# Performance work log

Hardware: AMD Instinct MI355X
Metric: run time of the kernel (lower is better)

Reference implementation:

```python
import jax, jax.numpy as jnp
import numpy as np
from functools import partial

B, N, T_HIST, T_FCST, HID, F, DEG = 16, 2000, 24, 24, 64, 8, 32
E_TOTAL = B * N * DEG


def setup_inputs() -> dict:
    key = jax.random.key(0)
    ks = jax.random.split(key, 20)
    s = 1.0 / np.sqrt(HID)
    # block-diagonal batched edge_index, as built by _process_adj_mat
    src = jax.random.randint(ks[0], (B, N * DEG), 0, N, dtype=jnp.int32)
    dst = jax.random.randint(ks[1], (B, N * DEG), 0, N, dtype=jnp.int32)
    off = (jnp.arange(B, dtype=jnp.int32) * N)[:, None]
    edge_index = jnp.stack([(src + off).reshape(-1), (dst + off).reshape(-1)], axis=0)
    return {
        "pm25_hist": jax.random.normal(ks[2], (B, T_HIST, N, 1), jnp.float32),
        "feature": jax.random.normal(ks[3], (B, T_HIST + T_FCST, N, F), jnp.float32),
        "edge_index": edge_index,
        "w_ih_enc": jax.random.normal(ks[4], (3 * HID, 2), jnp.float32) * s,
        "w_hh_enc": jax.random.normal(ks[5], (3 * HID, HID), jnp.float32) * s,
        "b_ih_enc": jnp.zeros((3 * HID,), jnp.float32),
        "b_hh_enc": jnp.zeros((3 * HID,), jnp.float32),
        "fc_w": jax.random.normal(ks[6], (1, HID), jnp.float32) * s,
        "fc_b": jnp.zeros((1,), jnp.float32),
        "cheb_w0": jax.random.normal(ks[7], (F + 1, 1), jnp.float32) * s,
        "cheb_w1": jax.random.normal(ks[8], (F + 1, 1), jnp.float32) * s,
        "cheb_b": jnp.zeros((1,), jnp.float32),
        "w_ih_dec": jax.random.normal(ks[9], (3 * HID, F + 2), jnp.float32) * s,
        "w_hh_dec": jax.random.normal(ks[10], (3 * HID, HID), jnp.float32) * s,
        "b_ih_dec": jnp.zeros((3 * HID,), jnp.float32),
        "b_hh_dec": jnp.zeros((3 * HID,), jnp.float32),
        "out_w": jax.random.normal(ks[11], (1, 2 * HID), jnp.float32) * s,
        "out_b": jnp.zeros((1,), jnp.float32),
    }


def gru(x, h, w_ih, w_hh, b_ih, b_hh):
    gi = x @ w_ih.T + b_ih
    gh = h @ w_hh.T + b_hh
    i_r, i_z, i_n = jnp.split(gi, 3, axis=-1)
    h_r, h_z, h_n = jnp.split(gh, 3, axis=-1)
    r = jax.nn.sigmoid(i_r + h_r)
    z = jax.nn.sigmoid(i_z + h_z)
    n = jnp.tanh(i_n + r * h_n)
    return (1.0 - z) * n + z * h


def cheb_conv(x, edge_index, w0, w1, b):
    # ChebConv K=2, sym norm, lambda_max=2 -> T1(L_hat) = -D^-1/2 A D^-1/2
    src, dst = edge_index[0], edge_index[1]
    ones = jnp.ones(src.shape, x.dtype)
    deg = jax.ops.segment_sum(ones, dst, num_segments=B * N)
    dis = jnp.where(deg > 0, jax.lax.rsqrt(jnp.maximum(deg, 1.0)), 0.0)
    norm = -(dis[src] * dis[dst])
    tx1 = jax.ops.segment_sum(norm[:, None] * x[src], dst, num_segments=B * N)
    return x @ w0 + tx1 @ w1 + b


def reference(pm25_hist, feature, edge_index, w_ih_enc, w_hh_enc, b_ih_enc, b_hh_enc,
              fc_w, fc_b, cheb_w0, cheb_w1, cheb_b, w_ih_dec, w_hh_dec, b_ih_dec,
              b_hh_dec, out_w, out_b):
    # ---------------- encoder ----------------
    h0 = jnp.zeros((B * N, HID), pm25_hist.dtype)
    x0 = jnp.zeros((B, N, 1), pm25_hist.dtype)

    def enc_step(carry, pm_t):
        hn, xn = carry
        x = jnp.concatenate([xn, pm_t], axis=-1).reshape(B * N, 2)
        hn = gru(x, hn, w_ih_enc, w_hh_enc, b_ih_enc, b_hh_enc)
        h3 = hn.reshape(B, N, HID)
        xn = h3 @ fc_w.T + fc_b
        return (hn, xn), h3

    (hn, xn), Hs = jax.lax.scan(enc_step, (h0, x0), pm25_hist.transpose(1, 0, 2, 3))
    H = Hs.transpose(1, 0, 2, 3)  # (B, T_HIST, N, HID)

    # ---------------- decoder ----------------
    def dec_step(carry, feat_t):
        hn, xn = carry
        x = jnp.concatenate([xn, feat_t], axis=-1)  # (B, N, F+1)
        xg = jax.nn.sigmoid(cheb_conv(x.reshape(B * N, F + 1), edge_index,
                                      cheb_w0, cheb_w1, cheb_b))
        x2 = jnp.concatenate([x, xg.reshape(B, N, 1)], axis=-1).reshape(B * N, F + 2)
        hn = gru(x2, hn, w_ih_dec, w_hh_dec, b_ih_dec, b_hh_dec)
        xn3 = hn.reshape(B, N, HID)
        energy = jnp.einsum('btnd,bnd->bnt', H, xn3)  # history attention
        alpha = jax.nn.softmax(energy, axis=2)
        a = jnp.einsum('bnt,btnd->bnd', alpha, H)
        xn = jnp.concatenate([a, xn3], axis=-1) @ out_w.T + out_b
        return (hn, xn), xn

    feats = feature[:, T_HIST:].transpose(1, 0, 2, 3)  # (T_FCST, B, N, F)
    _, preds = jax.lax.scan(dec_step, (hn, xn), feats)
    return preds.transpose(1, 0, 2, 3)  # (B, T_FCST, N, 1)
```

## Files before the change

kernel.cpp:

```cpp
#include <hip/hip_runtime.h>
#include <hip/hip_bf16.h>
#include <cstddef>
#include <cstdint>

constexpr int NB    = 16;
constexpr int NN    = 2000;
constexpr int TH    = 24;
constexpr int TF    = 24;
constexpr int HID   = 64;
constexpr int NF    = 8;
constexpr int NODES = NB * NN;
constexpr int ETOT  = NODES * 32;
constexpr int TT    = TH + TF;
constexpr int BLKN  = 64;
constexpr int NBLK  = NODES / BLKN;

typedef __attribute__((ext_vector_type(8))) short bf16x8;
typedef __attribute__((ext_vector_type(4))) float f32x4;
typedef uint16_t u16;

__device__ __forceinline__ float sigmoidf_(float x) { return 1.f / (1.f + __expf(-x)); }
__device__ __forceinline__ float tanhf_(float x) {
    float e = __expf(2.f * x);
    return 1.f - 2.f / (e + 1.f);
}
__device__ __forceinline__ u16 bfh(float x) {
    __hip_bfloat16 b = __float2bfloat16(x);
    u16 u; __builtin_memcpy(&u, &b, 2); return u;
}
__device__ __forceinline__ float bff(u16 u) { return __uint_as_float(((uint32_t)u) << 16); }
__device__ __forceinline__ uint32_t pk(u16 a, u16 b) { return (uint32_t)a | ((uint32_t)b << 16); }

__global__ void k_init(float* __restrict__ dis) {
    int i = blockIdx.x * blockDim.x + threadIdx.x;
    if (i < NODES) dis[i] = 0.f;
}

__global__ void k_deg(const int* __restrict__ ei, float* __restrict__ deg) {
    int e = blockIdx.x * blockDim.x + threadIdx.x;
    if (e < ETOT) atomicAdd(&deg[ei[ETOT + e]], 1.0f);
}

__global__ __launch_bounds__(256) void k_scan(const float* __restrict__ degf,
                                              int* __restrict__ row0,
                                              int* __restrict__ cnt)
{
    __shared__ int part[256];
    const int tid = threadIdx.x;
    const int per = NODES / 256;
    const int base = tid * per;
    int s = 0;
    for (int i = 0; i < per; i++) s += (int)degf[base + i];
    part[tid] = s;
    __syncthreads();
    for (int off = 1; off < 256; off <<= 1) {
        int v = (tid >= off) ? part[tid - off] : 0;
        __syncthreads();
        part[tid] += v;
        __syncthreads();
    }
    int run = (tid == 0) ? 0 : part[tid - 1];
    for (int i = 0; i < per; i++) {
        row0[base + i] = run;
        cnt[base + i]  = 0;
        run += (int)degf[base + i];
    }
    if (tid == 255) row0[NODES] = run;
}

__global__ void k_dis(float* __restrict__ dis) {
    int i = blockIdx.x * blockDim.x + threadIdx.x;
    if (i < NODES) {
        float d = dis[i];
        dis[i] = (d > 0.f) ? rsqrtf(fmaxf(d, 1.f)) : 0.f;
    }
}

__global__ void k_fill(const int* __restrict__ ei, const float* __restrict__ dis,
                       const int* __restrict__ row0, int* __restrict__ cnt,
                       int2* __restrict__ edge8)
{
    int e = blockIdx.x * blockDim.x + threadIdx.x;
    if (e < ETOT) {
        int s = ei[e];
        int d = ei[ETOT + e];
        float nv = -(dis[s] * dis[d]);
        int p = atomicAdd(&cnt[d], 1);
        edge8[row0[d] + p] = make_int2(s, __float_as_int(nv));
    }
}

__global__ void k_prepE(const float* __restrict__ whe, const float* __restrict__ fcw,
                        u16* __restrict__ AH, u16* __restrict__ AL)
{
    int i = blockIdx.x * blockDim.x + threadIdx.x;
    if (i < 208 * 64) {
        int r = i >> 6, k = i & 63;
        float v = (r < 192) ? whe[r * 64 + k] : ((r == 192) ? fcw[k] : 0.f);
        u16 hi = bfh(v);
        AH[i] = hi;
        AL[i] = bfh(v - bff(hi));
    }
}

__global__ void k_prepD(const float* __restrict__ whd, const float* __restrict__ wihd,
                        u16* __restrict__ AH, u16* __restrict__ AL)
{
    int i = blockIdx.x * blockDim.x + threadIdx.x;
    if (i < 256 * 96) {
        int r = i / 96, k = i - r * 96;
        float v = 0.f;
        if (k < 64) {
            if (r < 192) v = whd[r * 64 + k];
        } else if (k < 74) {
            int xi = k - 64;
            if (r < 128)       v = wihd[r * 10 + xi];
            else if (r >= 192) v = wihd[(r - 64) * 10 + xi];
        }
        u16 hi = bfh(v);
        AH[i] = hi;
        AL[i] = bfh(v - bff(hi));
    }
}

__global__ __launch_bounds__(256, 2) void k_encM(
    const float* __restrict__ pm, const u16* __restrict__ AeH, const u16* __restrict__ AeL,
    const float* __restrict__ w_ih, const float* __restrict__ b_ih, const float* __restrict__ b_hh,
    const float* __restrict__ fc_b, const float* __restrict__ feat, const float* __restrict__ cw1,
    u16* __restrict__ BgH, u16* __restrict__ BgL, u16* __restrict__ Hb,
    float* __restrict__ xn_buf, float* __restrict__ y1)
{
    __shared__ u16 BH[2][64 * 64], BL[2][64 * 64];
    __shared__ float pmL[TH * BLKN];
    __shared__ float xnL[BLKN];

    const int tid = threadIdx.x;
    const int l   = tid & 63;
    const int wv  = __builtin_amdgcn_readfirstlane(tid >> 6);
    const int n0  = blockIdx.x * BLKN;
    const int cn  = l & 15;
    const int kg  = l >> 4;
    const int c0  = wv * 16 + kg * 4;

    for (int i = tid; i < 64 * 64 / 2; i += 256) {
        ((uint32_t*)BH[0])[i] = 0u;
        ((uint32_t*)BL[0])[i] = 0u;
    }
    for (int i = tid; i < TH * BLKN; i += 256) {
        int t = i >> 6, n = i & 63;
        int node = n0 + n, b = node / NN, nn2 = node - b * NN;
        pmL[i] = pm[(b * TH + t) * NN + nn2];
    }
    bf16x8 AHf[4][2], ALf[4][2];
    #pragma unroll
    for (int s = 0; s < 4; s++) {
        #pragma unroll
        for (int ks = 0; ks < 2; ks++) {
            bf16x8 zh = {0,0,0,0,0,0,0,0};
            AHf[s][ks] = zh; ALf[s][ks] = zh;
            if (s < 3 || wv == 0) {
                int row = (wv + 4 * s) * 16 + cn;
                int off = row * 64 + ks * 32 + kg * 8;
                AHf[s][ks] = *(const bf16x8*)(AeH + off);
                ALf[s][ks] = *(const bf16x8*)(AeL + off);
            }
        }
    }
    float bR[4], bZ[4], biN[4], bhN[4];
    float wR0[4], wR1[4], wZ0[4], wZ1[4], wN0[4], wN1[4];
    #pragma unroll
    for (int j = 0; j < 4; j++) {
        int c = c0 + j;
        bR[j]  = b_ih[c] + b_hh[c];
        bZ[j]  = b_ih[64 + c] + b_hh[64 + c];
        biN[j] = b_ih[128 + c];
        bhN[j] = b_hh[128 + c];
        wR0[j] = w_ih[2 * c];           wR1[j] = w_ih[2 * c + 1];
        wZ0[j] = w_ih[2 * (64 + c)];    wZ1[j] = w_ih[2 * (64 + c) + 1];
        wN0[j] = w_ih[2 * (128 + c)];   wN1[j] = w_ih[2 * (128 + c) + 1];
    }
    const float fcb = fc_b[0];
    __syncthreads();

    for (int t = 0; t < TH; t++) {
        const int cur = t & 1, nxt = cur ^ 1;
        f32x4 acc[4][4];
        #pragma unroll
        for (int s = 0; s < 4; s++)
            #pragma unroll
            for (int ct = 0; ct < 4; ct++)
                acc[s][ct] = (f32x4){0.f, 0.f, 0.f, 0.f};

        #pragma unroll
        for (int ct = 0; ct < 4; ct++) {
            const int n = ct * 16 + cn;
            #pragma unroll
            for (int ks = 0; ks < 2; ks++) {
                const int idx = (n * 64 + ks * 32 + kg * 8) ^ ((n & 7) << 3);
                bf16x8 bh = *(const bf16x8*)&BH[cur][idx];
                bf16x8 bl = *(const bf16x8*)&BL[cur][idx];
                #pragma unroll
                for (int s = 0; s < 4; s++) {
                    if (s < 3 || wv == 0) {
                        acc[s][ct] = __builtin_amdgcn_mfma_f32_16x16x32_bf16(AHf[s][ks], bh, acc[s][ct], 0, 0, 0);
                        acc[s][ct] = __builtin_amdgcn_mfma_f32_16x16x32_bf16(AHf[s][ks], bl, acc[s][ct], 0, 0, 0);
                        acc[s][ct] = __builtin_amdgcn_mfma_f32_16x16x32_bf16(ALf[s][ks], bh, acc[s][ct], 0, 0, 0);
                    }
                }
            }
        }
        if (wv == 0 && kg == 0) {
            #pragma unroll
            for (int ct = 0; ct < 4; ct++) xnL[ct * 16 + cn] = acc[3][ct][0];
        }
        __syncthreads();

        #pragma unroll
        for (int ct = 0; ct < 4; ct++) {
            const int n = ct * 16 + cn, node = n0 + n;
            float xn = 0.f;
            if (t > 0) xn = xnL[n] + fcb;
            const float pv = pmL[t * 64 + n];
            const int hidx = (n * 64 + c0) ^ ((n & 7) << 3);
            uint2 oh = *(const uint2*)&BH[cur][hidx];
            uint2 ol = *(const uint2*)&BL[cur][hidx];
            float hnew[4];
            #pragma unroll
            for (int j = 0; j < 4; j++) {
                u16 hh = (j < 2) ? (u16)((j == 0) ? (oh.x & 0xffff) : (oh.x >> 16))
                                 : (u16)((j == 2) ? (oh.y & 0xffff) : (oh.y >> 16));
                u16 ll = (j < 2) ? (u16)((j == 0) ? (ol.x & 0xffff) : (ol.x >> 16))
                                 : (u16)((j == 2) ? (ol.y & 0xffff) : (ol.y >> 16));
                float hold = bff(hh) + bff(ll);
                float r  = sigmoidf_(acc[0][ct][j] + bR[j] + wR0[j] * xn + wR1[j] * pv);
                float z  = sigmoidf_(acc[1][ct][j] + bZ[j] + wZ0[j] * xn + wZ1[j] * pv);
                float gi = biN[j] + wN0[j] * xn + wN1[j] * pv;
                float gh = acc[2][ct][j] + bhN[j];
                float nn_ = tanhf_(gi + r * gh);
                hnew[j] = (1.f - z) * nn_ + z * hold;
            }
            u16 nh0 = bfh(hnew[0]), nh1 = bfh(hnew[1]), nh2 = bfh(hnew[2]), nh3 = bfh(hnew[3]);
            u16 nl0 = bfh(hnew[0] - bff(nh0)), nl1 = bfh(hnew[1] - bff(nh1));
            u16 nl2 = bfh(hnew[2] - bff(nh2)), nl3 = bfh(hnew[3] - bff(nh3));
            uint2 ph = make_uint2(pk(nh0, nh1), pk(nh2, nh3));
            uint2 pl = make_uint2(pk(nl0, nl1), pk(nl2, nl3));
            *(uint2*)&BH[nxt][hidx] = ph;
            *(uint2*)&BL[nxt][hidx] = pl;
            *(uint2*)(Hb + (size_t)node * (TH * HID) + t * HID + c0) = ph;
        }
        __syncthreads();
    }

    if (wv == 0) {
        f32x4 ax[4];
        #pragma unroll
        for (int ct = 0; ct < 4; ct++) ax[ct] = (f32x4){0.f, 0.f, 0.f, 0.f};
        #pragma unroll
        for (int ct = 0; ct < 4; ct++) {
            const int n = ct * 16 + cn;
            #pragma unroll
            for (int ks = 0; ks < 2; ks++) {
                const int idx = (n * 64 + ks * 32 + kg * 8) ^ ((n & 7) << 3);
                bf16x8 bh = *(const bf16x8*)&BH[0][idx];
                bf16x8 bl = *(const bf16x8*)&BL[0][idx];
                ax[ct] = __builtin_amdgcn_mfma_f32_16x16x32_bf16(AHf[3][ks], bh, ax[ct], 0, 0, 0);
                ax[ct] = __builtin_amdgcn_mfma_f32_16x16x32_bf16(AHf[3][ks], bl, ax[ct], 0, 0, 0);
                ax[ct] = __builtin_amdgcn_mfma_f32_16x16x32_bf16(ALf[3][ks], bh, ax[ct], 0, 0, 0);
            }
        }
        if (kg == 0) {
            #pragma unroll
            for (int ct = 0; ct < 4; ct++) xnL[ct * 16 + cn] = ax[ct][0];
        }
    }
    __syncthreads();

    for (int i = tid; i < 512; i += 256) {
        int n = i >> 3, sl = i & 7;
        int idx = (n * 64 + sl * 8) ^ ((n & 7) << 3);
        *(uint4*)(BgH + ((size_t)(n0 + n)) * 64 + sl * 8) = *(const uint4*)&BH[0][idx];
        *(uint4*)(BgL + ((size_t)(n0 + n)) * 64 + sl * 8) = *(const uint4*)&BL[0][idx];
    }
    if (tid < BLKN) {
        int n = tid, node = n0 + n;
        float xv = xnL[n] + fcb;
        xn_buf[node] = xv;
        int b = node / NN, nn2 = node - b * NN;
        const float* fp = feat + ((size_t)(b * TT + TH) * NN + nn2) * NF;
        float yy = xv * cw1[0];
        #pragma unroll
        for (int q = 0; q < NF; q++) yy += fp[q] * cw1[1 + q];
        y1[node] = yy;
    }
}

__global__ __launch_bounds__(256) void k_gather(
    const int* __restrict__ row0, const int2* __restrict__ edge8,
    const float* __restrict__ y1, float* __restrict__ tx)
{
    const int tid  = blockIdx.x * 256 + threadIdx.x;
    const int node = tid >> 2;
    const int q    = tid & 3;
    if (node >= NODES) return;
    const int beg = row0[node], end = row0[node + 1];
    float acc = 0.f;
    for (int i = beg + q; i < end; i += 4) {
        const int2 e = edge8[i];
        acc = fmaf(__int_as_float(e.y), y1[e.x], acc);
    }
    acc += __shfl_xor(acc, 1, 64);
    acc += __shfl_xor(acc, 2, 64);
    if (q == 0) tx[node] = acc;
}

__global__ __launch_bounds__(256, 2) void k_decM(
    const float* __restrict__ feat, const u16* __restrict__ AdH, const u16* __restrict__ AdL,
    const float* __restrict__ b_ih, const float* __restrict__ b_hh,
    const float* __restrict__ w0, const float* __restrict__ cb,
    const float* __restrict__ xn_buf, const float* __restrict__ tx,
    const u16* __restrict__ BgHin, const u16* __restrict__ BgLin,
    u16* __restrict__ BgHout, u16* __restrict__ BgLout, int t)
{
    __shared__ u16 XH[64 * 96], XL[64 * 96];
    const int tid = threadIdx.x;
    const int l   = tid & 63;
    const int wv  = __builtin_amdgcn_readfirstlane(tid >> 6);
    const int n0  = blockIdx.x * BLKN;
    const int cn  = l & 15, kg = l >> 4;
    const int c0  = wv * 16 + kg * 4;

    for (int i = tid; i < 512; i += 256) {
        int n = i >> 3, sl = i & 7;
        int idx = (n * 96 + sl * 8) ^ ((n & 7) << 3);
        *(uint4*)&XH[idx] = *(const uint4*)(BgHin + ((size_t)(n0 + n)) * 64 + sl * 8);
        *(uint4*)&XL[idx] = *(const uint4*)(BgLin + ((size_t)(n0 + n)) * 64 + sl * 8);
    }
    if (tid < BLKN) {
        int n = tid, node = n0 + n;
        int b = node / NN, nn2 = node - b * NN;
        float x0 = xn_buf[node];
        const float* fp = feat + ((size_t)(b * TT + TH + t) * NN + nn2) * NF;
        float f0 = fp[0], f1 = fp[1], f2 = fp[2], f3 = fp[3];
        float f4 = fp[4], f5 = fp[5], f6 = fp[6], f7 = fp[7];
        float xw = x0 * w0[0];
        xw = fmaf(f0, w0[1], xw); xw = fmaf(f1, w0[2], xw);
        xw = fmaf(f2, w0[3], xw); xw = fmaf(f3, w0[4], xw);
        xw = fmaf(f4, w0[5], xw); xw = fmaf(f5, w0[6], xw);
        xw = fmaf(f6, w0[7], xw); xw = fmaf(f7, w0[8], xw);
        float xg = sigmoidf_(xw + tx[node] + cb[0]);
        u16 h0 = bfh(x0), h1 = bfh(f0), h2 = bfh(f1), h3 = bfh(f2), h4 = bfh(f3);
        u16 h5 = bfh(f4), h6 = bfh(f5), h7 = bfh(f6), h8 = bfh(f7), h9 = bfh(xg);
        u16 l0 = bfh(x0 - bff(h0)), l1 = bfh(f0 - bff(h1)), l2 = bfh(f1 - bff(h2));
        u16 l3 = bfh(f2 - bff(h3)), l4 = bfh(f3 - bff(h4)), l5 = bfh(f4 - bff(h5));
        u16 l6 = bfh(f5 - bff(h6)), l7 = bfh(f6 - bff(h7)), l8 = bfh(f7 - bff(h8));
        u16 l9 = bfh(xg - bff(h9));
        uint4 qh0 = make_uint4(pk(h0, h1), pk(h2, h3), pk(h4, h5), pk(h6, h7));
        uint4 qh1 = make_uint4(pk(h8, h9), 0u, 0u, 0u);
        uint4 ql0 = make_uint4(pk(l0, l1), pk(l2, l3), pk(l4, l5), pk(l6, l7));
        uint4 ql1 = make_uint4(pk(l8, l9), 0u, 0u, 0u);
        uint4 zz  = make_uint4(0u, 0u, 0u, 0u);
        const int sw = (n & 7) << 3;
        *(uint4*)&XH[(n * 96 + 64) ^ sw] = qh0;
        *(uint4*)&XH[(n * 96 + 72) ^ sw] = qh1;
        *(uint4*)&XH[(n * 96 + 80) ^ sw] = zz;
        *(uint4*)&XH[(n * 96 + 88) ^ sw] = zz;
        *(uint4*)&XL[(n * 96 + 64) ^ sw] = ql0;
        *(uint4*)&XL[(n * 96 + 72) ^ sw] = ql1;
        *(uint4*)&XL[(n * 96 + 80) ^ sw] = zz;
        *(uint4*)&XL[(n * 96 + 88) ^ sw] = zz;
    }
    float bsR[4], bsZ[4], biN[4], bhN[4];
    #pragma unroll
    for (int j = 0; j < 4; j++) {
        int c = c0 + j;
        bsR[j] = b_ih[c] + b_hh[c];
        bsZ[j] = b_ih[64 + c] + b_hh[64 + c];
        biN[j] = b_ih[128 + c];
        bhN[j] = b_hh[128 + c];
    }
    bf16x8 AHf[4][3], ALf[4][3];
    #pragma unroll
    for (int s = 0; s < 4; s++) {
        #pragma unroll
        for (int ks = 0; ks < 3; ks++) {
            bf16x8 zh = {0,0,0,0,0,0,0,0};
            AHf[s][ks] = zh; ALf[s][ks] = zh;
            const bool live = (s < 2) || (s == 2 && ks < 2) || (s == 3 && ks == 2);
            if (live) {
                int row = (wv + 4 * s) * 16 + cn;
                int off = row * 96 + ks * 32 + kg * 8;
                AHf[s][ks] = *(const bf16x8*)(AdH + off);
                ALf[s][ks] = *(const bf16x8*)(AdL + off);
            }
        }
    }
    __syncthreads();

    f32x4 acc[4][4];
    #pragma unroll
    for (int s = 0; s < 4; s++)
        #pragma unroll
        for (int ct = 0; ct < 4; ct++)
            acc[s][ct] = (f32x4){0.f, 0.f, 0.f, 0.f};

    #pragma unroll
    for (int ct = 0; ct < 4; ct++) {
        const int n = ct * 16 + cn;
        #pragma unroll
        for (int ks = 0; ks < 3; ks++) {
            const int idx = (n * 96 + ks * 32 + kg * 8) ^ ((n & 7) << 3);
            bf16x8 bh = *(const bf16x8*)&XH[idx];
            bf16x8 bl = *(const bf16x8*)&XL[idx];
            #pragma unroll
            for (int s = 0; s < 4; s++) {
                const bool live = (s < 2) || (s == 2 && ks < 2) || (s == 3 && ks == 2);
                if (live) {
                    acc[s][ct] = __builtin_amdgcn_mfma_f32_16x16x32_bf16(AHf[s][ks], bh, acc[s][ct], 0, 0, 0);
                    acc[s][ct] = __builtin_amdgcn_mfma_f32_16x16x32_bf16(AHf[s][ks], bl, acc[s][ct], 0, 0, 0);
                    acc[s][ct] = __builtin_amdgcn_mfma_f32_16x16x32_bf16(ALf[s][ks], bh, acc[s][ct], 0, 0, 0);
                }
            }
        }
    }

    #pragma unroll
    for (int ct = 0; ct < 4; ct++) {
        const int n = ct * 16 + cn, node = n0 + n;
        const int hidx = (n * 96 + c0) ^ ((n & 7) << 3);
        uint2 oh = *(const uint2*)&XH[hidx];
        uint2 ol = *(const uint2*)&XL[hidx];
        float hnew[4];
        #pragma unroll
        for (int j = 0; j < 4; j++) {
            u16 hh = (j < 2) ? (u16)((j == 0) ? (oh.x & 0xffff) : (oh.x >> 16))
                             : (u16)((j == 2) ? (oh.y & 0xffff) : (oh.y >> 16));
            u16 ll = (j < 2) ? (u16)((j == 0) ? (ol.x & 0xffff) : (ol.x >> 16))
                             : (u16)((j == 2) ? (ol.y & 0xffff) : (ol.y >> 16));
            float hold = bff(hh) + bff(ll);
            float r  = sigmoidf_(acc[0][ct][j] + bsR[j]);
            float z  = sigmoidf_(acc[1][ct][j] + bsZ[j]);
            float nn_ = tanhf_((acc[3][ct][j] + biN[j]) + r * (acc[2][ct][j] + bhN[j]));
            hnew[j] = (1.f - z) * nn_ + z * hold;
        }
        u16 nh0 = bfh(hnew[0]), nh1 = bfh(hnew[1]), nh2 = bfh(hnew[2]), nh3 = bfh(hnew[3]);
        u16 nl0 = bfh(hnew[0] - bff(nh0)), nl1 = bfh(hnew[1] - bff(nh1));
        u16 nl2 = bfh(hnew[2] - bff(nh2)), nl3 = bfh(hnew[3] - bff(nh3));
        *(uint2*)(BgHout + (size_t)node * 64 + c0) = make_uint2(pk(nh0, nh1), pk(nh2, nh3));
        *(uint2*)(BgLout + (size_t)node * 64 + c0) = make_uint2(pk(nl0, nl1), pk(nl2, nl3));
    }
}

__global__ __launch_bounds__(256) void k_attn(
    const u16* __restrict__ Hb, const u16* __restrict__ BgH, const u16* __restrict__ BgL,
    const float* __restrict__ out_w, const float* __restrict__ out_b,
    const float* __restrict__ feat, const float* __restrict__ cw1,
    float* __restrict__ xn_buf, float* __restrict__ y1,
    float* __restrict__ out, int t)
{
    const int wid  = threadIdx.x >> 6;
    const int lane = threadIdx.x & 63;
    const int node = blockIdx.x * 4 + wid;
    if (node >= NODES) return;
    const int d0 = (lane & 7) * 8;

    const float hj = bff(BgH[(size_t)node * 64 + lane]) + bff(BgL[(size_t)node * 64 + lane]);
    float hval[8];
    #pragma unroll
    for (int q = 0; q < 8; q++) hval[q] = __shfl(hj, d0 + q, 64);

    const uint4* Hrow = (const uint4*)(Hb + (size_t)node * (TH * HID));
    float Hf[3][8];
    float er[3];
    #pragma unroll
    for (int R = 0; R < 3; R++) {
        const uint4 v = Hrow[R * 64 + lane];
        const uint32_t u0 = v.x, u1 = v.y, u2 = v.z, u3 = v.w;
        Hf[R][0] = __uint_as_float(u0 << 16);
        Hf[R][1] = __uint_as_float(u0 & 0xffff0000u);
        Hf[R][2] = __uint_as_float(u1 << 16);
        Hf[R][3] = __uint_as_float(u1 & 0xffff0000u);
        Hf[R][4] = __uint_as_float(u2 << 16);
        Hf[R][5] = __uint_as_float(u2 & 0xffff0000u);
        Hf[R][6] = __uint_as_float(u3 << 16);
        Hf[R][7] = __uint_as_float(u3 & 0xffff0000u);
        float part = 0.f;
        #pragma unroll
        for (int q = 0; q < 8; q++) part = fmaf(Hf[R][q], hval[q], part);
        part += __shfl_xor(part, 1, 64);
        part += __shfl_xor(part, 2, 64);
        part += __shfl_xor(part, 4, 64);
        er[R] = part;
    }

    float m = fmaxf(fmaxf(er[0], er[1]), er[2]);
    m = fmaxf(m, __shfl_xor(m, 8, 64));
    m = fmaxf(m, __shfl_xor(m, 16, 64));
    m = fmaxf(m, __shfl_xor(m, 32, 64));

    float w0_ = __expf(er[0] - m);
    float w1_ = __expf(er[1] - m);
    float w2_ = __expf(er[2] - m);
    float s = w0_ + w1_ + w2_;
    s += __shfl_xor(s, 8, 64);
    s += __shfl_xor(s, 16, 64);
    s += __shfl_xor(s, 32, 64);
    const float rs = 1.f / s;

    float aq[8];
    #pragma unroll
    for (int q = 0; q < 8; q++) {
        float a = w0_ * Hf[0][q];
        a = fmaf(w1_, Hf[1][q], a);
        a = fmaf(w2_, Hf[2][q], a);
        a += __shfl_xor(a, 8, 64);
        a += __shfl_xor(a, 16, 64);
        a += __shfl_xor(a, 32, 64);
        aq[q] = a * rs;
    }

    float part = 0.f;
    #pragma unroll
    for (int q = 0; q < 8; q++) {
        part = fmaf(out_w[d0 + q],       aq[q],   part);
        part = fmaf(out_w[HID + d0 + q], hval[q], part);
    }
    part += __shfl_xor(part, 1, 64);
    part += __shfl_xor(part, 2, 64);
    part += __shfl_xor(part, 4, 64);
    const float xnew = part + out_b[0];

    if (lane == 0) {
        const int b = node / NN, n = node - b * NN;
        out[(b * TF + t) * NN + n] = xnew;
        xn_buf[node] = xnew;
        if (t + 1 < TF) {
            const float* fp = feat + ((size_t)(b * TT + TH + t + 1) * NN + n) * NF;
            float yy = xnew * cw1[0];
            #pragma unroll
            for (int c = 0; c < NF; c++) yy += fp[c] * cw1[1 + c];
            y1[node] = yy;
        }
    }
}

extern "C" void kernel_launch(void* const* d_in, const int* in_sizes, int n_in,
                              void* d_out, int out_size, void* d_ws, size_t ws_size,
                              hipStream_t stream)
{
    const float* pm     = (const float*)d_in[0];
    const float* feat   = (const float*)d_in[1];
    const int*   ei     = (const int*)d_in[2];
    const float* w_ih_e = (const float*)d_in[3];
    const float* w_hh_e = (const float*)d_in[4];
    const float* b_ih_e = (const float*)d_in[5];
    const float* b_hh_e = (const float*)d_in[6];
    const float* fc_w   = (const float*)d_in[7];
    const float* fc_b   = (const float*)d_in[8];
    const float* cw0    = (const float*)d_in[9];
    const float* cw1    = (const float*)d_in[10];
    const float* cb     = (const float*)d_in[11];
    const float* w_ih_d = (const float*)d_in[12];
    const float* w_hh_d = (const float*)d_in[13];
    const float* b_ih_d = (const float*)d_in[14];
    const float* b_hh_d = (const float*)d_in[15];
    const float* out_w  = (const float*)d_in[16];
    const float* out_b  = (const float*)d_in[17];
    float* out = (float*)d_out;

    char* ws = (char*)d_ws;
    size_t off = 0;
    auto alloc = [&](size_t bytes) -> void* {
        void* p = ws + off;
        off += (bytes + 255) & ~(size_t)255;
        return p;
    };
    u16* Hb    = (u16*)alloc(sizeof(u16) * (size_t)NODES * TH * HID);
    u16* BgAH  = (u16*)alloc(sizeof(u16) * (size_t)NODES * HID);
    u16* BgAL  = (u16*)alloc(sizeof(u16) * (size_t)NODES * HID);
    u16* BgBH  = (u16*)alloc(sizeof(u16) * (size_t)NODES * HID);
    u16* BgBL  = (u16*)alloc(sizeof(u16) * (size_t)NODES * HID);
    float* xn  = (float*)alloc(sizeof(float) * NODES);
    float* dis = (float*)alloc(sizeof(float) * NODES);
    float* y1  = (float*)alloc(sizeof(float) * NODES);
    float* tx  = (float*)alloc(sizeof(float) * NODES);
    u16* AeH   = (u16*)alloc(sizeof(u16) * 208 * 64);
    u16* AeL   = (u16*)alloc(sizeof(u16) * 208 * 64);
    u16* AdH   = (u16*)alloc(sizeof(u16) * 256 * 96);
    u16* AdL   = (u16*)alloc(sizeof(u16) * 256 * 96);
    int* row0  = (int*)alloc(sizeof(int) * (NODES + 1));
    int* cnt   = (int*)alloc(sizeof(int) * NODES);
    int2* edge8 = (int2*)alloc(sizeof(int2) * ETOT);
    if (off > ws_size) return;

    k_init<<<(NODES + 255) / 256, 256, 0, stream>>>(dis);
    k_deg<<<(ETOT + 255) / 256, 256, 0, stream>>>(ei, dis);
    k_scan<<<1, 256, 0, stream>>>(dis, row0, cnt);
    k_dis<<<(NODES + 255) / 256, 256, 0, stream>>>(dis);
    k_fill<<<(ETOT + 255) / 256, 256, 0, stream>>>(ei, dis, row0, cnt, edge8);
    k_prepE<<<(208 * 64 + 255) / 256, 256, 0, stream>>>(w_hh_e, fc_w, AeH, AeL);
    k_prepD<<<(256 * 96 + 255) / 256, 256, 0, stream>>>(w_hh_d, w_ih_d, AdH, AdL);

    k_encM<<<NBLK, 256, 0, stream>>>(pm, AeH, AeL, w_ih_e, b_ih_e, b_hh_e,
                                     fc_b, feat, cw1, BgAH, BgAL, Hb, xn, y1);

    for (int t = 0; t < TF; t++) {
        const u16* inH = (t & 1) ? BgBH : BgAH;
        const u16* inL = (t & 1) ? BgBL : BgAL;
        u16* outH      = (t & 1) ? BgAH : BgBH;
        u16* outL      = (t & 1) ? BgAL : BgBL;
        k_gather<<<(NODES * 4) / 256, 256, 0, stream>>>(row0, edge8, y1, tx);
        k_decM<<<NBLK, 256, 0, stream>>>(feat, AdH, AdL, b_ih_d, b_hh_d,
                                         cw0, cb, xn, tx, inH, inL, outH, outL, t);
        k_attn<<<NODES / 4, 256, 0, stream>>>(Hb, outH, outL, out_w, out_b, feat, cw1,
                                              xn, y1, out, t);
    }
}
```

Baseline: 1.202 ms.

## Fuse gather, decoder GRU and attention into one per-step kernel; shrink encoder blocks

```diff
diff --git a/kernel.cpp b/kernel.cpp
--- a/kernel.cpp
+++ b/kernel.cpp
@@ -12,8 +12,10 @@
 constexpr int NODES = NB * NN;
 constexpr int ETOT  = NODES * 32;
 constexpr int TT    = TH + TF;
-constexpr int BLKN  = 64;
-constexpr int NBLK  = NODES / BLKN;
+constexpr int EBLK  = 32;
+constexpr int NEBLK = NODES / EBLK;
+constexpr int DBLK  = 64;
+constexpr int NDBLK = NODES / DBLK;
 
 typedef __attribute__((ext_vector_type(8))) short bf16x8;
 typedef __attribute__((ext_vector_type(4))) float f32x4;
@@ -123,31 +125,31 @@
     }
 }
 
-__global__ __launch_bounds__(256, 2) void k_encM(
+__global__ __launch_bounds__(256, 4) void k_encM(
     const float* __restrict__ pm, const u16* __restrict__ AeH, const u16* __restrict__ AeL,
     const float* __restrict__ w_ih, const float* __restrict__ b_ih, const float* __restrict__ b_hh,
     const float* __restrict__ fc_b, const float* __restrict__ feat, const float* __restrict__ cw1,
     u16* __restrict__ BgH, u16* __restrict__ BgL, u16* __restrict__ Hb,
     float* __restrict__ xn_buf, float* __restrict__ y1)
 {
-    __shared__ u16 BH[2][64 * 64], BL[2][64 * 64];
-    __shared__ float pmL[TH * BLKN];
-    __shared__ float xnL[BLKN];
+    __shared__ u16 BH[2][EBLK * 64], BL[2][EBLK * 64];
+    __shared__ float pmL[TH * EBLK];
+    __shared__ float xnL[EBLK];
 
     const int tid = threadIdx.x;
     const int l   = tid & 63;
     const int wv  = __builtin_amdgcn_readfirstlane(tid >> 6);
-    const int n0  = blockIdx.x * BLKN;
+    const int n0  = blockIdx.x * EBLK;
     const int cn  = l & 15;
     const int kg  = l >> 4;
     const int c0  = wv * 16 + kg * 4;
 
-    for (int i = tid; i < 64 * 64 / 2; i += 256) {
+    for (int i = tid; i < EBLK * 64 / 2; i += 256) {
         ((uint32_t*)BH[0])[i] = 0u;
         ((uint32_t*)BL[0])[i] = 0u;
     }
-    for (int i = tid; i < TH * BLKN; i += 256) {
-        int t = i >> 6, n = i & 63;
+    for (int i = tid; i < TH * EBLK; i += 256) {
+        int t = i >> 5, n = i & 31;
         int node = n0 + n, b = node / NN, nn2 = node - b * NN;
         pmL[i] = pm[(b * TH + t) * NN + nn2];
     }
@@ -180,25 +182,33 @@
         wN0[j] = w_ih[2 * (128 + c)];   wN1[j] = w_ih[2 * (128 + c) + 1];
     }
     const float fcb = fc_b[0];
+    int baddr[2][2], haddr[2];
+    #pragma unroll
+    for (int ct = 0; ct < 2; ct++) {
+        const int n = ct * 16 + cn;
+        #pragma unroll
+        for (int ks = 0; ks < 2; ks++)
+            baddr[ct][ks] = (n * 64 + ks * 32 + kg * 8) ^ ((n & 7) << 3);
+        haddr[ct] = (n * 64 + c0) ^ ((n & 7) << 3);
+    }
+    float hreg[2][4] = {{0.f,0.f,0.f,0.f},{0.f,0.f,0.f,0.f}};
     __syncthreads();
 
     for (int t = 0; t < TH; t++) {
         const int cur = t & 1, nxt = cur ^ 1;
-        f32x4 acc[4][4];
+        f32x4 acc[4][2];
         #pragma unroll
         for (int s = 0; s < 4; s++)
             #pragma unroll
-            for (int ct = 0; ct < 4; ct++)
+            for (int ct = 0; ct < 2; ct++)
                 acc[s][ct] = (f32x4){0.f, 0.f, 0.f, 0.f};
 
         #pragma unroll
-        for (int ct = 0; ct < 4; ct++) {
-            const int n = ct * 16 + cn;
+        for (int ct = 0; ct < 2; ct++) {
             #pragma unroll
             for (int ks = 0; ks < 2; ks++) {
-                const int idx = (n * 64 + ks * 32 + kg * 8) ^ ((n & 7) << 3);
-                bf16x8 bh = *(const bf16x8*)&BH[cur][idx];
-                bf16x8 bl = *(const bf16x8*)&BL[cur][idx];
+                bf16x8 bh = *(const bf16x8*)&BH[cur][baddr[ct][ks]];
+                bf16x8 bl = *(const bf16x8*)&BL[cur][baddr[ct][ks]];
                 #pragma unroll
                 for (int s = 0; s < 4; s++) {
                     if (s < 3 || wv == 0) {
@@ -211,58 +221,49 @@
         }
         if (wv == 0 && kg == 0) {
             #pragma unroll
-            for (int ct = 0; ct < 4; ct++) xnL[ct * 16 + cn] = acc[3][ct][0];
+            for (int ct = 0; ct < 2; ct++) xnL[ct * 16 + cn] = acc[3][ct][0];
         }
         __syncthreads();
 
         #pragma unroll
-        for (int ct = 0; ct < 4; ct++) {
+        for (int ct = 0; ct < 2; ct++) {
             const int n = ct * 16 + cn, node = n0 + n;
             float xn = 0.f;
             if (t > 0) xn = xnL[n] + fcb;
-            const float pv = pmL[t * 64 + n];
-            const int hidx = (n * 64 + c0) ^ ((n & 7) << 3);
-            uint2 oh = *(const uint2*)&BH[cur][hidx];
-            uint2 ol = *(const uint2*)&BL[cur][hidx];
+            const float pv = pmL[t * EBLK + n];
             float hnew[4];
             #pragma unroll
             for (int j = 0; j < 4; j++) {
-                u16 hh = (j < 2) ? (u16)((j == 0) ? (oh.x & 0xffff) : (oh.x >> 16))
-                                 : (u16)((j == 2) ? (oh.y & 0xffff) : (oh.y >> 16));
-                u16 ll = (j < 2) ? (u16)((j == 0) ? (ol.x & 0xffff) : (ol.x >> 16))
-                                 : (u16)((j == 2) ? (ol.y & 0xffff) : (ol.y >> 16));
-                float hold = bff(hh) + bff(ll);
                 float r  = sigmoidf_(acc[0][ct][j] + bR[j] + wR0[j] * xn + wR1[j] * pv);
                 float z  = sigmoidf_(acc[1][ct][j] + bZ[j] + wZ0[j] * xn + wZ1[j] * pv);
                 float gi = biN[j] + wN0[j] * xn + wN1[j] * pv;
                 float gh = acc[2][ct][j] + bhN[j];
                 float nn_ = tanhf_(gi + r * gh);
-                hnew[j] = (1.f - z) * nn_ + z * hold;
+                hnew[j] = (1.f - z) * nn_ + z * hreg[ct][j];
+                hreg[ct][j] = hnew[j];
             }
             u16 nh0 = bfh(hnew[0]), nh1 = bfh(hnew[1]), nh2 = bfh(hnew[2]), nh3 = bfh(hnew[3]);
             u16 nl0 = bfh(hnew[0] - bff(nh0)), nl1 = bfh(hnew[1] - bff(nh1));
             u16 nl2 = bfh(hnew[2] - bff(nh2)), nl3 = bfh(hnew[3] - bff(nh3));
             uint2 ph = make_uint2(pk(nh0, nh1), pk(nh2, nh3));
             uint2 pl = make_uint2(pk(nl0, nl1), pk(nl2, nl3));
-            *(uint2*)&BH[nxt][hidx] = ph;
-            *(uint2*)&BL[nxt][hidx] = pl;
+            *(uint2*)&BH[nxt][haddr[ct]] = ph;
+            *(uint2*)&BL[nxt][haddr[ct]] = pl;
             *(uint2*)(Hb + (size_t)node * (TH * HID) + t * HID + c0) = ph;
         }
         __syncthreads();
     }
 
     if (wv == 0) {
-        f32x4 ax[4];
-        #pragma unroll
-        for (int ct = 0; ct < 4; ct++) ax[ct] = (f32x4){0.f, 0.f, 0.f, 0.f};
-        #pragma unroll
-        for (int ct = 0; ct < 4; ct++) {
-            const int n = ct * 16 + cn;
+        f32x4 ax[2];
+        #pragma unroll
+        for (int ct = 0; ct < 2; ct++) ax[ct] = (f32x4){0.f, 0.f, 0.f, 0.f};
+        #pragma unroll
+        for (int ct = 0; ct < 2; ct++) {
             #pragma unroll
             for (int ks = 0; ks < 2; ks++) {
-                const int idx = (n * 64 + ks * 32 + kg * 8) ^ ((n & 7) << 3);
-                bf16x8 bh = *(const bf16x8*)&BH[0][idx];
-                bf16x8 bl = *(const bf16x8*)&BL[0][idx];
+                bf16x8 bh = *(const bf16x8*)&BH[0][baddr[ct][ks]];
+                bf16x8 bl = *(const bf16x8*)&BL[0][baddr[ct][ks]];
                 ax[ct] = __builtin_amdgcn_mfma_f32_16x16x32_bf16(AHf[3][ks], bh, ax[ct], 0, 0, 0);
                 ax[ct] = __builtin_amdgcn_mfma_f32_16x16x32_bf16(AHf[3][ks], bl, ax[ct], 0, 0, 0);
                 ax[ct] = __builtin_amdgcn_mfma_f32_16x16x32_bf16(ALf[3][ks], bh, ax[ct], 0, 0, 0);
@@ -270,18 +271,18 @@
         }
         if (kg == 0) {
             #pragma unroll
-            for (int ct = 0; ct < 4; ct++) xnL[ct * 16 + cn] = ax[ct][0];
+            for (int ct = 0; ct < 2; ct++) xnL[ct * 16 + cn] = ax[ct][0];
         }
     }
     __syncthreads();
 
-    for (int i = tid; i < 512; i += 256) {
-        int n = i >> 3, sl = i & 7;
+    {
+        int n = tid >> 3, sl = tid & 7;
         int idx = (n * 64 + sl * 8) ^ ((n & 7) << 3);
         *(uint4*)(BgH + ((size_t)(n0 + n)) * 64 + sl * 8) = *(const uint4*)&BH[0][idx];
         *(uint4*)(BgL + ((size_t)(n0 + n)) * 64 + sl * 8) = *(const uint4*)&BL[0][idx];
     }
-    if (tid < BLKN) {
+    if (tid < EBLK) {
         int n = tid, node = n0 + n;
         float xv = xnL[n] + fcb;
         xn_buf[node] = xv;
@@ -294,50 +295,77 @@
     }
 }
 
-__global__ __launch_bounds__(256) void k_gather(
-    const int* __restrict__ row0, const int2* __restrict__ edge8,
-    const float* __restrict__ y1, float* __restrict__ tx)
-{
-    const int tid  = blockIdx.x * 256 + threadIdx.x;
-    const int node = tid >> 2;
-    const int q    = tid & 3;
-    if (node >= NODES) return;
-    const int beg = row0[node], end = row0[node + 1];
-    float acc = 0.f;
-    for (int i = beg + q; i < end; i += 4) {
-        const int2 e = edge8[i];
-        acc = fmaf(__int_as_float(e.y), y1[e.x], acc);
-    }
-    acc += __shfl_xor(acc, 1, 64);
-    acc += __shfl_xor(acc, 2, 64);
-    if (q == 0) tx[node] = acc;
-}
-
-__global__ __launch_bounds__(256, 2) void k_decM(
+__global__ __launch_bounds__(256, 2) void k_decF(
     const float* __restrict__ feat, const u16* __restrict__ AdH, const u16* __restrict__ AdL,
     const float* __restrict__ b_ih, const float* __restrict__ b_hh,
     const float* __restrict__ w0, const float* __restrict__ cb,
-    const float* __restrict__ xn_buf, const float* __restrict__ tx,
+    float* __restrict__ xn_buf, const float* __restrict__ y1_in, float* __restrict__ y1_out,
+    const int* __restrict__ row0, const int2* __restrict__ edge8,
     const u16* __restrict__ BgHin, const u16* __restrict__ BgLin,
-    u16* __restrict__ BgHout, u16* __restrict__ BgLout, int t)
+    u16* __restrict__ BgHout, u16* __restrict__ BgLout,
+    const u16* __restrict__ Hb, const float* __restrict__ out_w, const float* __restrict__ out_b,
+    const float* __restrict__ cw1, float* __restrict__ out, int t)
 {
     __shared__ u16 XH[64 * 96], XL[64 * 96];
+    __shared__ float gpart[4][DBLK];
+    __shared__ float hx[DBLK][68];
+
     const int tid = threadIdx.x;
     const int l   = tid & 63;
     const int wv  = __builtin_amdgcn_readfirstlane(tid >> 6);
-    const int n0  = blockIdx.x * BLKN;
+    const int n0  = blockIdx.x * DBLK;
     const int cn  = l & 15, kg = l >> 4;
     const int c0  = wv * 16 + kg * 4;
 
+    {
+        const int na = tid >> 2;
+        const int q  = tid & 3;
+        const int nd = n0 + na;
+        const int beg = row0[nd], end = row0[nd + 1];
+        float acc = 0.f;
+        for (int i = beg + q; i < end; i += 4) {
+            const int2 e = edge8[i];
+            acc = fmaf(__int_as_float(e.y), y1_in[e.x], acc);
+        }
+        gpart[q][na] = acc;
+    }
     for (int i = tid; i < 512; i += 256) {
         int n = i >> 3, sl = i & 7;
         int idx = (n * 96 + sl * 8) ^ ((n & 7) << 3);
         *(uint4*)&XH[idx] = *(const uint4*)(BgHin + ((size_t)(n0 + n)) * 64 + sl * 8);
         *(uint4*)&XL[idx] = *(const uint4*)(BgLin + ((size_t)(n0 + n)) * 64 + sl * 8);
     }
-    if (tid < BLKN) {
+    bf16x8 AHf[4][3], ALf[4][3];
+    #pragma unroll
+    for (int s = 0; s < 4; s++) {
+        #pragma unroll
+        for (int ks = 0; ks < 3; ks++) {
+            bf16x8 zh = {0,0,0,0,0,0,0,0};
+            AHf[s][ks] = zh; ALf[s][ks] = zh;
+            const bool live = (s < 2) || (s == 2 && ks < 2) || (s == 3 && ks == 2);
+            if (live) {
+                int row = (wv + 4 * s) * 16 + cn;
+                int off = row * 96 + ks * 32 + kg * 8;
+                AHf[s][ks] = *(const bf16x8*)(AdH + off);
+                ALf[s][ks] = *(const bf16x8*)(AdL + off);
+            }
+        }
+    }
+    float bsR[4], bsZ[4], biN[4], bhN[4];
+    #pragma unroll
+    for (int j = 0; j < 4; j++) {
+        int c = c0 + j;
+        bsR[j] = b_ih[c] + b_hh[c];
+        bsZ[j] = b_ih[64 + c] + b_hh[64 + c];
+        biN[j] = b_ih[128 + c];
+        bhN[j] = b_hh[128 + c];
+    }
+    __syncthreads();
+
+    if (tid < DBLK) {
         int n = tid, node = n0 + n;
         int b = node / NN, nn2 = node - b * NN;
+        float txv = gpart[0][n] + gpart[1][n] + gpart[2][n] + gpart[3][n];
         float x0 = xn_buf[node];
         const float* fp = feat + ((size_t)(b * TT + TH + t) * NN + nn2) * NF;
         float f0 = fp[0], f1 = fp[1], f2 = fp[2], f3 = fp[3];
@@ -347,7 +375,7 @@
         xw = fmaf(f2, w0[3], xw); xw = fmaf(f3, w0[4], xw);
         xw = fmaf(f4, w0[5], xw); xw = fmaf(f5, w0[6], xw);
         xw = fmaf(f6, w0[7], xw); xw = fmaf(f7, w0[8], xw);
-        float xg = sigmoidf_(xw + tx[node] + cb[0]);
+        float xg = sigmoidf_(xw + txv + cb[0]);
         u16 h0 = bfh(x0), h1 = bfh(f0), h2 = bfh(f1), h3 = bfh(f2), h4 = bfh(f3);
         u16 h5 = bfh(f4), h6 = bfh(f5), h7 = bfh(f6), h8 = bfh(f7), h9 = bfh(xg);
         u16 l0 = bfh(x0 - bff(h0)), l1 = bfh(f0 - bff(h1)), l2 = bfh(f1 - bff(h2));
@@ -369,31 +397,6 @@
         *(uint4*)&XL[(n * 96 + 80) ^ sw] = zz;
         *(uint4*)&XL[(n * 96 + 88) ^ sw] = zz;
     }
-    float bsR[4], bsZ[4], biN[4], bhN[4];
-    #pragma unroll
-    for (int j = 0; j < 4; j++) {
-        int c = c0 + j;
-        bsR[j] = b_ih[c] + b_hh[c];
-        bsZ[j] = b_ih[64 + c] + b_hh[64 + c];
-        biN[j] = b_ih[128 + c];
-        bhN[j] = b_hh[128 + c];
-    }
-    bf16x8 AHf[4][3], ALf[4][3];
-    #pragma unroll
-    for (int s = 0; s < 4; s++) {
-        #pragma unroll
-        for (int ks = 0; ks < 3; ks++) {
-            bf16x8 zh = {0,0,0,0,0,0,0,0};
-            AHf[s][ks] = zh; ALf[s][ks] = zh;
-            const bool live = (s < 2) || (s == 2 && ks < 2) || (s == 3 && ks == 2);
-            if (live) {
-                int row = (wv + 4 * s) * 16 + cn;
-                int off = row * 96 + ks * 32 + kg * 8;
-                AHf[s][ks] = *(const bf16x8*)(AdH + off);
-                ALf[s][ks] = *(const bf16x8*)(AdL + off);
-            }
-        }
-    }
     __syncthreads();
 
     f32x4 acc[4][4];
@@ -447,98 +450,91 @@
         u16 nl2 = bfh(hnew[2] - bff(nh2)), nl3 = bfh(hnew[3] - bff(nh3));
         *(uint2*)(BgHout + (size_t)node * 64 + c0) = make_uint2(pk(nh0, nh1), pk(nh2, nh3));
         *(uint2*)(BgLout + (size_t)node * 64 + c0) = make_uint2(pk(nl0, nl1), pk(nl2, nl3));
-    }
-}
-
-__global__ __launch_bounds__(256) void k_attn(
-    const u16* __restrict__ Hb, const u16* __restrict__ BgH, const u16* __restrict__ BgL,
-    const float* __restrict__ out_w, const float* __restrict__ out_b,
-    const float* __restrict__ feat, const float* __restrict__ cw1,
-    float* __restrict__ xn_buf, float* __restrict__ y1,
-    float* __restrict__ out, int t)
-{
-    const int wid  = threadIdx.x >> 6;
-    const int lane = threadIdx.x & 63;
-    const int node = blockIdx.x * 4 + wid;
-    if (node >= NODES) return;
+        *(float4*)&hx[n][c0] = make_float4(hnew[0], hnew[1], hnew[2], hnew[3]);
+    }
+    __syncthreads();
+
+    const int lane = l;
     const int d0 = (lane & 7) * 8;
-
-    const float hj = bff(BgH[(size_t)node * 64 + lane]) + bff(BgL[(size_t)node * 64 + lane]);
-    float hval[8];
-    #pragma unroll
-    for (int q = 0; q < 8; q++) hval[q] = __shfl(hj, d0 + q, 64);
-
-    const uint4* Hrow = (const uint4*)(Hb + (size_t)node * (TH * HID));
-    float Hf[3][8];
-    float er[3];
-    #pragma unroll
-    for (int R = 0; R < 3; R++) {
-        const uint4 v = Hrow[R * 64 + lane];
-        const uint32_t u0 = v.x, u1 = v.y, u2 = v.z, u3 = v.w;
-        Hf[R][0] = __uint_as_float(u0 << 16);
-        Hf[R][1] = __uint_as_float(u0 & 0xffff0000u);
-        Hf[R][2] = __uint_as_float(u1 << 16);
-        Hf[R][3] = __uint_as_float(u1 & 0xffff0000u);
-        Hf[R][4] = __uint_as_float(u2 << 16);
-        Hf[R][5] = __uint_as_float(u2 & 0xffff0000u);
-        Hf[R][6] = __uint_as_float(u3 << 16);
-        Hf[R][7] = __uint_as_float(u3 & 0xffff0000u);
+    for (int r = 0; r < 16; r++) {
+        const int nl = wv * 16 + r;
+        const int node = n0 + nl;
+        float4 hv0 = *(const float4*)&hx[nl][d0];
+        float4 hv1 = *(const float4*)&hx[nl][d0 + 4];
+        float hval[8] = {hv0.x, hv0.y, hv0.z, hv0.w, hv1.x, hv1.y, hv1.z, hv1.w};
+
+        const uint4* Hrow = (const uint4*)(Hb + (size_t)node * (TH * HID));
+        float Hf[3][8];
+        float er[3];
+        #pragma unroll
+        for (int R = 0; R < 3; R++) {
+            const uint4 v = Hrow[R * 64 + lane];
+            const uint32_t u0 = v.x, u1 = v.y, u2 = v.z, u3 = v.w;
+            Hf[R][0] = __uint_as_float(u0 << 16);
+            Hf[R][1] = __uint_as_float(u0 & 0xffff0000u);
+            Hf[R][2] = __uint_as_float(u1 << 16);
+            Hf[R][3] = __uint_as_float(u1 & 0xffff0000u);
+            Hf[R][4] = __uint_as_float(u2 << 16);
+            Hf[R][5] = __uint_as_float(u2 & 0xffff0000u);
+            Hf[R][6] = __uint_as_float(u3 << 16);
+            Hf[R][7] = __uint_as_float(u3 & 0xffff0000u);
+            float part = 0.f;
+            #pragma unroll
+            for (int q = 0; q < 8; q++) part = fmaf(Hf[R][q], hval[q], part);
+            part += __shfl_xor(part, 1, 64);
+            part += __shfl_xor(part, 2, 64);
+            part += __shfl_xor(part, 4, 64);
+            er[R] = part;
+        }
+
+        float m = fmaxf(fmaxf(er[0], er[1]), er[2]);
+        m = fmaxf(m, __shfl_xor(m, 8, 64));
+        m = fmaxf(m, __shfl_xor(m, 16, 64));
+        m = fmaxf(m, __shfl_xor(m, 32, 64));
+
+        float w0_ = __expf(er[0] - m);
+        float w1_ = __expf(er[1] - m);
+        float w2_ = __expf(er[2] - m);
+        float s = w0_ + w1_ + w2_;
+        s += __shfl_xor(s, 8, 64);
+        s += __shfl_xor(s, 16, 64);
+        s += __shfl_xor(s, 32, 64);
+        const float rs = 1.f / s;
+
+        float aq[8];
+        #pragma unroll
+        for (int q = 0; q < 8; q++) {
+            float a = w0_ * Hf[0][q];
+            a = fmaf(w1_, Hf[1][q], a);
+            a = fmaf(w2_, Hf[2][q], a);
+            a += __shfl_xor(a, 8, 64);
+            a += __shfl_xor(a, 16, 64);
+            a += __shfl_xor(a, 32, 64);
+            aq[q] = a * rs;
+        }
+
         float part = 0.f;
         #pragma unroll
-        for (int q = 0; q < 8; q++) part = fmaf(Hf[R][q], hval[q], part);
+        for (int q = 0; q < 8; q++) {
+            part = fmaf(out_w[d0 + q],       aq[q],   part);
+            part = fmaf(out_w[HID + d0 + q], hval[q], part);
+        }
         part += __shfl_xor(part, 1, 64);
         part += __shfl_xor(part, 2, 64);
         part += __shfl_xor(part, 4, 64);
-        er[R] = part;
-    }
-
-    float m = fmaxf(fmaxf(er[0], er[1]), er[2]);
-    m = fmaxf(m, __shfl_xor(m, 8, 64));
-    m = fmaxf(m, __shfl_xor(m, 16, 64));
-    m = fmaxf(m, __shfl_xor(m, 32, 64));
-
-    float w0_ = __expf(er[0] - m);
-    float w1_ = __expf(er[1] - m);
-    float w2_ = __expf(er[2] - m);
-    float s = w0_ + w1_ + w2_;
-    s += __shfl_xor(s, 8, 64);
-    s += __shfl_xor(s, 16, 64);
-    s += __shfl_xor(s, 32, 64);
-    const float rs = 1.f / s;
-
-    float aq[8];
-    #pragma unroll
-    for (int q = 0; q < 8; q++) {
-        float a = w0_ * Hf[0][q];
-        a = fmaf(w1_, Hf[1][q], a);
-        a = fmaf(w2_, Hf[2][q], a);
-        a += __shfl_xor(a, 8, 64);
-        a += __shfl_xor(a, 16, 64);
-        a += __shfl_xor(a, 32, 64);
-        aq[q] = a * rs;
-    }
-
-    float part = 0.f;
-    #pragma unroll
-    for (int q = 0; q < 8; q++) {
-        part = fmaf(out_w[d0 + q],       aq[q],   part);
-        part = fmaf(out_w[HID + d0 + q], hval[q], part);
-    }
-    part += __shfl_xor(part, 1, 64);
-    part += __shfl_xor(part, 2, 64);
-    part += __shfl_xor(part, 4, 64);
-    const float xnew = part + out_b[0];
-
-    if (lane == 0) {
-        const int b = node / NN, n = node - b * NN;
-        out[(b * TF + t) * NN + n] = xnew;
-        xn_buf[node] = xnew;
-        if (t + 1 < TF) {
-            const float* fp = feat + ((size_t)(b * TT + TH + t + 1) * NN + n) * NF;
-            float yy = xnew * cw1[0];
-            #pragma unroll
-            for (int c = 0; c < NF; c++) yy += fp[c] * cw1[1 + c];
-            y1[node] = yy;
+        const float xnew = part + out_b[0];
+
+        if (lane == 0) {
+            const int b = node / NN, n = node - b * NN;
+            out[(b * TF + t) * NN + n] = xnew;
+            xn_buf[node] = xnew;
+            if (t + 1 < TF) {
+                const float* fp = feat + ((size_t)(b * TT + TH + t + 1) * NN + n) * NF;
+                float yy = xnew * cw1[0];
+                #pragma unroll
+                for (int c = 0; c < NF; c++) yy += fp[c] * cw1[1 + c];
+                y1_out[node] = yy;
+            }
         }
     }
 }
@@ -581,8 +577,8 @@
     u16* BgBL  = (u16*)alloc(sizeof(u16) * (size_t)NODES * HID);
     float* xn  = (float*)alloc(sizeof(float) * NODES);
     float* dis = (float*)alloc(sizeof(float) * NODES);
-    float* y1  = (float*)alloc(sizeof(float) * NODES);
-    float* tx  = (float*)alloc(sizeof(float) * NODES);
+    float* y1A = (float*)alloc(sizeof(float) * NODES);
+    float* y1B = (float*)alloc(sizeof(float) * NODES);
     u16* AeH   = (u16*)alloc(sizeof(u16) * 208 * 64);
     u16* AeL   = (u16*)alloc(sizeof(u16) * 208 * 64);
     u16* AdH   = (u16*)alloc(sizeof(u16) * 256 * 96);
@@ -600,18 +596,19 @@
     k_prepE<<<(208 * 64 + 255) / 256, 256, 0, stream>>>(w_hh_e, fc_w, AeH, AeL);
     k_prepD<<<(256 * 96 + 255) / 256, 256, 0, stream>>>(w_hh_d, w_ih_d, AdH, AdL);
 
-    k_encM<<<NBLK, 256, 0, stream>>>(pm, AeH, AeL, w_ih_e, b_ih_e, b_hh_e,
-                                     fc_b, feat, cw1, BgAH, BgAL, Hb, xn, y1);
+    k_encM<<<NEBLK, 256, 0, stream>>>(pm, AeH, AeL, w_ih_e, b_ih_e, b_hh_e,
+                                      fc_b, feat, cw1, BgAH, BgAL, Hb, xn, y1A);
 
     for (int t = 0; t < TF; t++) {
         const u16* inH = (t & 1) ? BgBH : BgAH;
         const u16* inL = (t & 1) ? BgBL : BgAL;
         u16* outH      = (t & 1) ? BgAH : BgBH;
         u16* outL      = (t & 1) ? BgAL : BgBL;
-        k_gather<<<(NODES * 4) / 256, 256, 0, stream>>>(row0, edge8, y1, tx);
-        k_decM<<<NBLK, 256, 0, stream>>>(feat, AdH, AdL, b_ih_d, b_hh_d,
-                                         cw0, cb, xn, tx, inH, inL, outH, outL, t);
-        k_attn<<<NODES / 4, 256, 0, stream>>>(Hb, outH, outL, out_w, out_b, feat, cw1,
-                                              xn, y1, out, t);
-    }
-}
+        const float* yin = (t & 1) ? y1B : y1A;
+        float* yout      = (t & 1) ? y1A : y1B;
+        k_decF<<<NDBLK, 256, 0, stream>>>(feat, AdH, AdL, b_ih_d, b_hh_d,
+                                          cw0, cb, xn, yin, yout, row0, edge8,
+                                          inH, inL, outH, outL,
+                                          Hb, out_w, out_b, cw1, out, t);
+    }
+}
```

After: 1.358 ms. 1.13x slower.
